# Performance work log

Measured on AMD Instinct MI355X. Metric: run time of the kernel, lower is better.

## Reference

```python
import jax, jax.numpy as jnp
import numpy as np
import math

HEAD = 4
B, N, C = 8, 1024, 256


def setup_inputs() -> dict:
    key = jax.random.key(0)
    k1, k2, k3, k4, k5 = jax.random.split(key, 5)
    query = jax.random.normal(k1, (B, N, C), dtype=jnp.float32)
    keyt = jax.random.normal(k2, (B, N, C), dtype=jnp.float32)
    value = jax.random.normal(k3, (B, N, C), dtype=jnp.float32)
    mask = jax.random.randint(k4, (B, N, N), 0, 2).astype(bool)
    dis = jax.random.normal(k5, (B, N, N), dtype=jnp.float32)
    return {"query": query, "key": keyt, "value": value, "mask": mask, "dis": dis}


def reference(query, key, value, mask, dis):
    Bq, Nq, Cq = key.shape
    d = Cq // HEAD
    # split heads: [B,N,C] -> [h,B,N,d]
    q = query.reshape(Bq, Nq, HEAD, d).transpose(2, 0, 1, 3)
    k = key.reshape(Bq, Nq, HEAD, d).transpose(2, 0, 1, 3)
    v = value.reshape(Bq, Nq, HEAD, d).transpose(2, 0, 1, 3)
    # scores: [h,B,N,N]; note: dis added BEFORE scaling, as in the torch code
    scores = jnp.einsum('hbnd,hbmd->hbnm', q, k)
    scores = scores + dis[None]            # dis broadcasts over head dim
    scores = scores / math.sqrt(d)
    scores = jnp.where(mask[None], -jnp.inf, scores)
    p_attn = jax.nn.softmax(scores, axis=-1)
    out = jnp.einsum('hbnm,hbmd->hbnd', p_attn, v)  # [h,B,N,d]
    out = out.transpose(1, 2, 0, 3).reshape(Bq, Nq, Cq)
    return out, p_attn
```

## Files before the change

### kernel.cpp

```cpp
#include <hip/hip_runtime.h>
#include <math.h>

#define HEADS 4
#define BATCH 8
#define SEQ   1024
#define CH    256
#define DH    64
#define RB    16
#define NTHR  512
#define SSTR  1032

typedef float  floatx4  __attribute__((ext_vector_type(4)));
typedef short  shortx8  __attribute__((ext_vector_type(8)));

__device__ __forceinline__ unsigned short f2bf(float f) {
    unsigned u = __float_as_uint(f);
    unsigned r = u + 0x7FFFu + ((u >> 16) & 1u);
    return (unsigned short)(r >> 16);
}
__device__ __forceinline__ float bf2f(unsigned short h) {
    return __uint_as_float(((unsigned)h) << 16);
}
__device__ __forceinline__ shortx8 pack8(float4 a, float4 b) {
    shortx8 r;
    r[0] = (short)f2bf(a.x); r[1] = (short)f2bf(a.y);
    r[2] = (short)f2bf(a.z); r[3] = (short)f2bf(a.w);
    r[4] = (short)f2bf(b.x); r[5] = (short)f2bf(b.y);
    r[6] = (short)f2bf(b.z); r[7] = (short)f2bf(b.w);
    return r;
}

__global__ __launch_bounds__(NTHR, 8)
void attn_mfma(const float* __restrict__ q, const float* __restrict__ k,
               const float* __restrict__ v, const void* __restrict__ maskp,
               const float* __restrict__ dis, float* __restrict__ out,
               float* __restrict__ pout)
{
    __shared__ unsigned short Sraw[RB][SSTR];
    __shared__ float Opart[RB][65];
    __shared__ float part[8][RB];
    __shared__ float invs[RB];

    const int t   = threadIdx.x;
    const int bid = blockIdx.x;
    const int nb  = bid & 63;
    const int hb  = bid >> 6;
    const int b   = hb & (BATCH - 1);
    const int h   = hb >> 3;
    const int n0  = nb * RB;

    const int lane = t & 63;
    const int w    = t >> 6;
    const int ln   = lane & 15;
    const int qd   = lane >> 4;

    int fl;
    {
        const unsigned* mw = (const unsigned*)maskp;
        int found = 0;
        #pragma unroll
        for (int j = 0; j < 16; ++j)
            if (mw[lane * 16 + j] & 0xFFFFFF00u) found = 1;
        fl = (__ballot(found != 0) != 0ULL) ? 1 : 0;
    }
    const unsigned char* mask8  = (const unsigned char*)maskp;
    const int*           mask32 = (const int*)maskp;

    const float* qrow = q + ((size_t)(b * SEQ + n0 + ln)) * CH + h * DH;
    shortx8 aq0, aq1;
    {
        float4 a0 = *(const float4*)(qrow + qd * 8);
        float4 a1 = *(const float4*)(qrow + qd * 8 + 4);
        float4 a2 = *(const float4*)(qrow + 32 + qd * 8);
        float4 a3 = *(const float4*)(qrow + 32 + qd * 8 + 4);
        aq0 = pack8(a0, a1);
        aq1 = pack8(a2, a3);
    }

    const float* kbase = k + ((size_t)(b * SEQ)) * CH + h * DH;
    const float* vbase = v + ((size_t)(b * SEQ)) * CH + h * DH;

    const size_t dib0 = ((size_t)(b * SEQ + n0 + qd * 4)) * SEQ + w * 16 + ln;
    float psum[4] = {0.f, 0.f, 0.f, 0.f};
    float dv[4]; int mk[4];
    #pragma unroll
    for (int r = 0; r < 4; ++r) {
        size_t di = dib0 + (size_t)r * SEQ;
        dv[r] = dis[di];
        mk[r] = fl ? (int)mask8[di] : mask32[di];
    }
    for (int mc = 0; mc < 8; ++mc) {
        const int mcn = (mc < 7) ? mc + 1 : 7;
        const size_t dibn = dib0 + (size_t)mcn * 128;
        float dvn[4]; int mkn[4];
        #pragma unroll
        for (int r = 0; r < 4; ++r) {
            size_t di = dibn + (size_t)r * SEQ;
            dvn[r] = dis[di];
            mkn[r] = fl ? (int)mask8[di] : mask32[di];
        }
        const int mg = mc * 128 + w * 16 + ln;
        const float* krow = kbase + (size_t)mg * CH;
        float4 k0 = *(const float4*)(krow + qd * 8);
        float4 k1 = *(const float4*)(krow + qd * 8 + 4);
        float4 k2 = *(const float4*)(krow + 32 + qd * 8);
        float4 k3 = *(const float4*)(krow + 32 + qd * 8 + 4);

        shortx8 b0 = pack8(k0, k1), b1 = pack8(k2, k3);
        floatx4 acc = {0.f, 0.f, 0.f, 0.f};
        acc = __builtin_amdgcn_mfma_f32_16x16x32_bf16(aq0, b0, acc, 0, 0, 0);
        acc = __builtin_amdgcn_mfma_f32_16x16x32_bf16(aq1, b1, acc, 0, 0, 0);
        #pragma unroll
        for (int r = 0; r < 4; ++r) {
            float ex = mk[r] ? 0.f : __expf((acc[r] + dv[r]) * 0.125f);
            psum[r] += ex;
            Sraw[qd * 4 + r][mg] = f2bf(ex);
        }
        #pragma unroll
        for (int r = 0; r < 4; ++r) { dv[r] = dvn[r]; mk[r] = mkn[r]; }
    }
    #pragma unroll
    for (int r = 0; r < 4; ++r) {
        float s = psum[r];
        #pragma unroll
        for (int m = 8; m; m >>= 1) s += __shfl_xor(s, m, 16);
        if (ln == 0) part[w][qd * 4 + r] = s;
    }
    __syncthreads();

    if (t < RB) {
        float s = 0.f;
        #pragma unroll
        for (int j = 0; j < 8; ++j) s += part[j][t];
        invs[t] = 1.0f / s;
    }
    __syncthreads();

    const int hm = w >> 2;
    const int c  = (w & 3) * 16;
    float* prow = pout + ((size_t)((h * BATCH + b) * SEQ + n0)) * SEQ;
    floatx4 acco = {0.f, 0.f, 0.f, 0.f};
    float vv[8];
    {
        const int kb0 = hm * 512 + qd * 8;
        #pragma unroll
        for (int j = 0; j < 8; ++j)
            vv[j] = vbase[(size_t)(kb0 + j) * CH + c + ln];
    }
    for (int st = 0; st < 16; ++st) {
        const int stn = (st < 15) ? st + 1 : 15;
        const int kbn = hm * 512 + stn * 32 + qd * 8;
        float vn[8];
        #pragma unroll
        for (int j = 0; j < 8; ++j)
            vn[j] = vbase[(size_t)(kbn + j) * CH + c + ln];
        {
            const float inv = invs[st];
            unsigned pk = *(const unsigned*)&Sraw[st][t * 2];
            float2 pv = { bf2f((unsigned short)(pk & 0xFFFFu)) * inv,
                          bf2f((unsigned short)(pk >> 16)) * inv };
            *(float2*)(prow + (size_t)st * SEQ + t * 2) = pv;
        }
        const int kb = hm * 512 + st * 32 + qd * 8;
        shortx8 af = *(const shortx8*)&Sraw[ln][kb];
        shortx8 bfv;
        #pragma unroll
        for (int j = 0; j < 8; ++j) bfv[j] = (short)f2bf(vv[j]);
        acco = __builtin_amdgcn_mfma_f32_16x16x32_bf16(af, bfv, acco, 0, 0, 0);
        #pragma unroll
        for (int j = 0; j < 8; ++j) vv[j] = vn[j];
    }
    if (hm == 1) {
        #pragma unroll
        for (int r = 0; r < 4; ++r) Opart[qd * 4 + r][c + ln] = acco[r];
    }
    __syncthreads();
    if (hm == 0) {
        #pragma unroll
        for (int r = 0; r < 4; ++r) {
            int row = qd * 4 + r;
            out[((size_t)(b * SEQ + n0 + row)) * CH + h * DH + c + ln]
                = (acco[r] + Opart[row][c + ln]) * invs[row];
        }
    }
}

extern "C" void kernel_launch(void* const* d_in, const int* in_sizes, int n_in,
                              void* d_out, int out_size, void* d_ws, size_t ws_size,
                              hipStream_t stream) {
    const float* q    = (const float*)d_in[0];
    const float* k    = (const float*)d_in[1];
    const float* v    = (const float*)d_in[2];
    const void*  mask = d_in[3];
    const float* dis  = (const float*)d_in[4];
    float* out  = (float*)d_out;
    float* pout = out + (size_t)BATCH * SEQ * CH;
    (void)d_ws; (void)ws_size;

    attn_mfma<<<HEADS * BATCH * (SEQ / RB), NTHR, 0, stream>>>(
        q, k, v, mask, dis, out, pout);
}
```

Baseline: 334.2 us.

## Stage dis and mask into LDS with coalesced vector loads before QK phase

The block's dis and mask rows are preloaded with coalesced float4/int4 loads, and the masked bias is stored as bf16 in the shared score buffer. Masked entries get -inf, so the exp loop no longer needs a per-element mask test. The P writeback moves to its own coalesced float4 loop after normalization, and the PV loop drops its manual V prefetch. The aim is to replace the scattered per-lane global loads of dis and mask with wide coalesced ones. In exchange, dis is rounded to bf16 before the add, which reduces accuracy, and the removed prefetch may expose V load latency.

```diff
diff --git a/kernel.cpp b/kernel.cpp
--- a/kernel.cpp
+++ b/kernel.cpp
@@ -12,6 +12,7 @@
 
 typedef float  floatx4  __attribute__((ext_vector_type(4)));
 typedef short  shortx8  __attribute__((ext_vector_type(8)));
+typedef unsigned short ushortx4 __attribute__((ext_vector_type(4)));
 
 __device__ __forceinline__ unsigned short f2bf(float f) {
     unsigned u = __float_as_uint(f);
@@ -66,6 +67,32 @@
     const unsigned char* mask8  = (const unsigned char*)maskp;
     const int*           mask32 = (const int*)maskp;
 
+    {
+        const float* disrow = dis + ((size_t)(b * SEQ + n0)) * SEQ;
+        const unsigned char* m8r  = mask8  + ((size_t)(b * SEQ + n0)) * SEQ;
+        const int*           m32r = mask32 + ((size_t)(b * SEQ + n0)) * SEQ;
+        #pragma unroll
+        for (int i = 0; i < 8; ++i) {
+            const int idx = t + NTHR * i;
+            const int row = idx >> 8, c4 = (idx & 255) * 4;
+            float4 dv4 = *(const float4*)(disrow + (size_t)row * SEQ + c4);
+            unsigned mkb;
+            if (fl) {
+                mkb = *(const unsigned*)(m8r + (size_t)row * SEQ + c4);
+            } else {
+                int4 mv = *(const int4*)(m32r + (size_t)row * SEQ + c4);
+                mkb = (mv.x ? 1u : 0u) | (mv.y ? 0x100u : 0u)
+                    | (mv.z ? 0x10000u : 0u) | (mv.w ? 0x1000000u : 0u);
+            }
+            ushortx4 o;
+            o[0] = (mkb & 0x000000FFu) ? 0xFF80u : f2bf(dv4.x);
+            o[1] = (mkb & 0x0000FF00u) ? 0xFF80u : f2bf(dv4.y);
+            o[2] = (mkb & 0x00FF0000u) ? 0xFF80u : f2bf(dv4.z);
+            o[3] = (mkb & 0xFF000000u) ? 0xFF80u : f2bf(dv4.w);
+            *(ushortx4*)&Sraw[row][c4] = o;
+        }
+    }
+
     const float* qrow = q + ((size_t)(b * SEQ + n0 + ln)) * CH + h * DH;
     shortx8 aq0, aq1;
     {
@@ -76,29 +103,13 @@
         aq0 = pack8(a0, a1);
         aq1 = pack8(a2, a3);
     }
+    __syncthreads();
 
     const float* kbase = k + ((size_t)(b * SEQ)) * CH + h * DH;
     const float* vbase = v + ((size_t)(b * SEQ)) * CH + h * DH;
 
-    const size_t dib0 = ((size_t)(b * SEQ + n0 + qd * 4)) * SEQ + w * 16 + ln;
     float psum[4] = {0.f, 0.f, 0.f, 0.f};
-    float dv[4]; int mk[4];
-    #pragma unroll
-    for (int r = 0; r < 4; ++r) {
-        size_t di = dib0 + (size_t)r * SEQ;
-        dv[r] = dis[di];
-        mk[r] = fl ? (int)mask8[di] : mask32[di];
-    }
     for (int mc = 0; mc < 8; ++mc) {
-        const int mcn = (mc < 7) ? mc + 1 : 7;
-        const size_t dibn = dib0 + (size_t)mcn * 128;
-        float dvn[4]; int mkn[4];
-        #pragma unroll
-        for (int r = 0; r < 4; ++r) {
-            size_t di = dibn + (size_t)r * SEQ;
-            dvn[r] = dis[di];
-            mkn[r] = fl ? (int)mask8[di] : mask32[di];
-        }
         const int mg = mc * 128 + w * 16 + ln;
         const float* krow = kbase + (size_t)mg * CH;
         float4 k0 = *(const float4*)(krow + qd * 8);
@@ -112,12 +123,11 @@
         acc = __builtin_amdgcn_mfma_f32_16x16x32_bf16(aq1, b1, acc, 0, 0, 0);
         #pragma unroll
         for (int r = 0; r < 4; ++r) {
-            float ex = mk[r] ? 0.f : __expf((acc[r] + dv[r]) * 0.125f);
+            float pre = bf2f(Sraw[qd * 4 + r][mg]);
+            float ex  = __expf((acc[r] + pre) * 0.125f);
             psum[r] += ex;
             Sraw[qd * 4 + r][mg] = f2bf(ex);
         }
-        #pragma unroll
-        for (int r = 0; r < 4; ++r) { dv[r] = dvn[r]; mk[r] = mkn[r]; }
     }
     #pragma unroll
     for (int r = 0; r < 4; ++r) {
@@ -136,39 +146,37 @@
     }
     __syncthreads();
 
+    {
+        float* prow = pout + ((size_t)((h * BATCH + b) * SEQ + n0)) * SEQ;
+        #pragma unroll
+        for (int i = 0; i < 8; ++i) {
+            const int idx = t + NTHR * i;
+            const int row = idx >> 8, c4 = (idx & 255) * 4;
+            ushortx4 sp = *(const ushortx4*)&Sraw[row][c4];
+            const float inv = invs[row];
+            float4 pv = { bf2f(sp[0]) * inv, bf2f(sp[1]) * inv,
+                          bf2f(sp[2]) * inv, bf2f(sp[3]) * inv };
+            *(float4*)(prow + (size_t)row * SEQ + c4) = pv;
+        }
+    }
+
     const int hm = w >> 2;
     const int c  = (w & 3) * 16;
-    float* prow = pout + ((size_t)((h * BATCH + b) * SEQ + n0)) * SEQ;
     floatx4 acco = {0.f, 0.f, 0.f, 0.f};
-    float vv[8];
-    {
-        const int kb0 = hm * 512 + qd * 8;
-        #pragma unroll
-        for (int j = 0; j < 8; ++j)
-            vv[j] = vbase[(size_t)(kb0 + j) * CH + c + ln];
-    }
-    for (int st = 0; st < 16; ++st) {
-        const int stn = (st < 15) ? st + 1 : 15;
-        const int kbn = hm * 512 + stn * 32 + qd * 8;
-        float vn[8];
-        #pragma unroll
-        for (int j = 0; j < 8; ++j)
-            vn[j] = vbase[(size_t)(kbn + j) * CH + c + ln];
-        {
-            const float inv = invs[st];
-            unsigned pk = *(const unsigned*)&Sraw[st][t * 2];
-            float2 pv = { bf2f((unsigned short)(pk & 0xFFFFu)) * inv,
-                          bf2f((unsigned short)(pk >> 16)) * inv };
-            *(float2*)(prow + (size_t)st * SEQ + t * 2) = pv;
-        }
-        const int kb = hm * 512 + st * 32 + qd * 8;
-        shortx8 af = *(const shortx8*)&Sraw[ln][kb];
-        shortx8 bfv;
-        #pragma unroll
-        for (int j = 0; j < 8; ++j) bfv[j] = (short)f2bf(vv[j]);
-        acco = __builtin_amdgcn_mfma_f32_16x16x32_bf16(af, bfv, acco, 0, 0, 0);
-        #pragma unroll
-        for (int j = 0; j < 8; ++j) vv[j] = vn[j];
+    for (int mc = 0; mc < 8; ++mc) {
+        #pragma unroll
+        for (int s = 0; s < 2; ++s) {
+            const int kb = hm * 512 + mc * 64 + s * 32 + qd * 8;
+            float vv[8];
+            #pragma unroll
+            for (int j = 0; j < 8; ++j)
+                vv[j] = vbase[(size_t)(kb + j) * CH + c + ln];
+            shortx8 af = *(const shortx8*)&Sraw[ln][kb];
+            shortx8 bfv;
+            #pragma unroll
+            for (int j = 0; j < 8; ++j) bfv[j] = (short)f2bf(vv[j]);
+            acco = __builtin_amdgcn_mfma_f32_16x16x32_bf16(af, bfv, acco, 0, 0, 0);
+        }
     }
     if (hm == 1) {
         #pragma unroll
```

After: 313.7 us. 1.07x faster.
